# Kernel optimization log

Measured on AMD Instinct MI355X. Metric: run time of the kernel, lower is better.

## Reference

```python
import jax, jax.numpy as jnp
import numpy as np

NEG = -9.0e15

def gat_layer(X, adj_mask, W, Wb, a1, a2, ab):
    # X: [N, Fin]; W: [Fin, Fout]; a1,a2: [Fout]; ab: scalar
    h = X @ W + Wb                                   # [N, Fout]
    # a([h_i || h_j]) = h_i@a1 + h_j@a2 + ab  (decomposition of concat+linear)
    e = jax.nn.leaky_relu((h @ a1)[:, None] + (h @ a2)[None, :] + ab,
                          negative_slope=0.2)        # [N, N]
    e = jnp.where(adj_mask, e, NEG)
    attn = jax.nn.softmax(e, axis=1)                 # [N, N]
    return jax.nn.elu(attn @ h)                      # [N, Fout]

def setup_inputs() -> dict:
    key = jax.random.key(0)
    ks = jax.random.split(key, 12)
    N, Fin, Fh, H, Fout = 4096, 512, 128, 4, 64
    X = jax.random.normal(ks[0], (N, Fin), dtype=jnp.float32)
    adjacency_matrix = jax.random.randint(ks[1], (N, N), 0, 2, dtype=jnp.int32)
    s_in = 1.0 / np.sqrt(Fin)
    s_a = 1.0 / np.sqrt(2 * Fh)
    W_h  = jax.random.uniform(ks[2], (H, Fin, Fh), jnp.float32, -s_in, s_in)
    b_h  = jax.random.uniform(ks[3], (H, Fh), jnp.float32, -s_in, s_in)
    a1_h = jax.random.uniform(ks[4], (H, Fh), jnp.float32, -s_a, s_a)
    a2_h = jax.random.uniform(ks[5], (H, Fh), jnp.float32, -s_a, s_a)
    ab_h = jax.random.uniform(ks[6], (H,), jnp.float32, -s_a, s_a)
    Fcat = H * Fh
    s_c = 1.0 / np.sqrt(Fcat)
    s_ao = 1.0 / np.sqrt(2 * Fout)
    W_o  = jax.random.uniform(ks[7], (Fcat, Fout), jnp.float32, -s_c, s_c)
    b_o  = jax.random.uniform(ks[8], (Fout,), jnp.float32, -s_c, s_c)
    a1_o = jax.random.uniform(ks[9], (Fout,), jnp.float32, -s_ao, s_ao)
    a2_o = jax.random.uniform(ks[10], (Fout,), jnp.float32, -s_ao, s_ao)
    ab_o = jax.random.uniform(ks[11], (), jnp.float32, -s_ao, s_ao)
    return {"X": X, "adjacency_matrix": adjacency_matrix,
            "W_h": W_h, "b_h": b_h, "a1_h": a1_h, "a2_h": a2_h, "ab_h": ab_h,
            "W_o": W_o, "b_o": b_o, "a1_o": a1_o, "a2_o": a2_o, "ab_o": ab_o}

def reference(X, adjacency_matrix, W_h, b_h, a1_h, a2_h, ab_h,
              W_o, b_o, a1_o, a2_o, ab_o):
    adj_mask = adjacency_matrix > 0
    # per-head attention layers, vmapped over heads
    heads = jax.vmap(gat_layer, in_axes=(None, None, 0, 0, 0, 0, 0))(
        X, adj_mask, W_h, b_h, a1_h, a2_h, ab_h)      # [H, N, Fh]
    H, N, Fh = heads.shape
    x = jnp.transpose(heads, (1, 0, 2)).reshape(N, H * Fh)  # concat along features
    x = gat_layer(x, adj_mask, W_o, b_o, a1_o, a2_o, ab_o)  # [N, Fout]
    return jax.nn.log_softmax(x, axis=1)
```

## Files before the change

### kernel.cpp

```cpp
#include <hip/hip_runtime.h>
#include <math.h>

#define NN 4096

using f32x4  = __attribute__((ext_vector_type(4))) float;
using bf16x4 = __attribute__((ext_vector_type(4))) __bf16;
using bf16x8 = __attribute__((ext_vector_type(8))) __bf16;

__device__ __forceinline__ void barrier_lgkm() {
    asm volatile("s_waitcnt lgkmcnt(0)\ns_barrier" ::: "memory");
}

template<int FH>
__device__ __forceinline__ void stage_tile(const __bf16* __restrict__ hgp,
                                           __bf16* dst, int tid) {
#pragma unroll
    for (int it = 0; it < FH / 32; it++) {
        int c = tid + it * 256;
        int f = c >> 3, sl = c & 7;
        int g = sl ^ (f & 7);
        __builtin_amdgcn_global_load_lds(
            (const __attribute__((address_space(1))) void*)(hgp + (size_t)f * NN + g * 8),
            (__attribute__((address_space(3))) void*)(dst + (size_t)c * 8), 16, 0, 0);
    }
}

__device__ __forceinline__ void stage_g(const __bf16* __restrict__ base, int ldk,
                                        __bf16* dst, int tid) {
#pragma unroll
    for (int it = 0; it < 2; it++) {
        int c = tid + it * 256;
        int f = c >> 3, sl = c & 7;
        int g = sl ^ (f & 7);
        __builtin_amdgcn_global_load_lds(
            (const __attribute__((address_space(1))) void*)(base + (size_t)f * ldk + g * 8),
            (__attribute__((address_space(3))) void*)(dst + (size_t)c * 8), 16, 0, 0);
    }
}

__global__ void pack_adj_kernel(const int* __restrict__ adj,
                                unsigned long long* __restrict__ bits) {
    int gw = (blockIdx.x * blockDim.x + threadIdx.x) >> 6;
    int lane = threadIdx.x & 63;
    int v = adj[(size_t)gw * 64 + lane];
    unsigned long long m = __ballot(v > 0);
    if (lane == 0) bits[gw] = m;
}

__global__ void prepack_kernel(const float* __restrict__ W_h, const float* __restrict__ b_h,
                               const float* __restrict__ W_o,
                               __bf16* __restrict__ Bt1, float* __restrict__ biasp,
                               __bf16* __restrict__ Bt2) {
    int idx = blockIdx.x * 256 + threadIdx.x;
    {
        int n = idx >> 9, k = idx & 511;
        int h = n >> 7, f = n & 127;
        Bt1[idx] = (__bf16)W_h[(size_t)h * 512 * 128 + k * 128 + f];
    }
    if (idx < 64 * 512) {
        int n = idx >> 9, k = idx & 511;
        Bt2[idx] = (__bf16)W_o[k * 64 + n];
    }
    if (idx < 512) biasp[idx] = b_h[idx];
}

__global__ void cast_bf16_kernel(const float* __restrict__ src, __bf16* __restrict__ dst) {
    int i = blockIdx.x * 256 + threadIdx.x;
    f32x4 v = *(const f32x4*)(src + (size_t)i * 4);
    bf16x4 o;
#pragma unroll
    for (int q = 0; q < 4; q++) o[q] = (__bf16)v[q];
    *(bf16x4*)(dst + (size_t)i * 4) = o;
}

__global__ __launch_bounds__(256) void gemm_fused_kernel(
    const __bf16* __restrict__ A, const __bf16* __restrict__ Bt,
    const float* __restrict__ bias,
    const float* __restrict__ a1, const float* __restrict__ a2,
    __bf16* __restrict__ Ht, float* __restrict__ s1, float* __restrict__ s2,
    int M, int N, int K)
{
    __shared__ __attribute__((aligned(16))) __bf16 As[2][64 * 64];
    __shared__ __attribute__((aligned(16))) __bf16 Bs[2][64 * 64];
    const int tid = threadIdx.x, w = tid >> 6, l = tid & 63, o = l >> 4, rl = l & 15;
    const int bm = blockIdx.y * 64, bn = blockIdx.x * 64;
    f32x4 acc[4] = {};
    stage_g(A + (size_t)bm * K, K, &As[0][0], tid);
    stage_g(Bt + (size_t)bn * K, K, &Bs[0][0], tid);
    const int KB = K / 64;
    for (int kb = 0; kb < KB; kb++) {
        int b = kb & 1;
        __syncthreads();
        if (kb + 1 < KB) {
            stage_g(A + (size_t)bm * K + (kb + 1) * 64, K, &As[b ^ 1][0], tid);
            stage_g(Bt + (size_t)bn * K + (kb + 1) * 64, K, &Bs[b ^ 1][0], tid);
        }
#pragma unroll
        for (int kt = 0; kt < 2; kt++) {
            int ra = w * 16 + rl;
            int cg = kt * 4 + o;
            bf16x8 af = *(const bf16x8*)(&As[b][(ra * 8 + (cg ^ (ra & 7))) * 8]);
#pragma unroll
            for (int nt = 0; nt < 4; nt++) {
                int rb = nt * 16 + rl;
                bf16x8 bfr = *(const bf16x8*)(&Bs[b][(rb * 8 + (cg ^ (rb & 7))) * 8]);
                acc[nt] = __builtin_amdgcn_mfma_f32_16x16x32_bf16(af, bfr, acc[nt], 0, 0, 0);
            }
        }
    }
    const int head = bn >> 7;
    const int row_base = bm + w * 16 + o * 4;
    float p1[4] = {0.f, 0.f, 0.f, 0.f}, p2[4] = {0.f, 0.f, 0.f, 0.f};
#pragma unroll
    for (int nt = 0; nt < 4; nt++) {
        int col = bn + nt * 16 + rl;
        float bv = bias[col];
        float a1v = a1[col], a2v = a2[col];
        bf16x4 hv;
#pragma unroll
        for (int r4 = 0; r4 < 4; r4++) {
            float h = acc[nt][r4] + bv;
            hv[r4] = (__bf16)h;
            p1[r4] += h * a1v;
            p2[r4] += h * a2v;
        }
        *(bf16x4*)(Ht + (size_t)col * M + row_base) = hv;
    }
#pragma unroll
    for (int r4 = 0; r4 < 4; r4++)
#pragma unroll
        for (int off = 1; off < 16; off <<= 1) {
            p1[r4] += __shfl_xor(p1[r4], off, 64);
            p2[r4] += __shfl_xor(p2[r4], off, 64);
        }
    if (rl == 0)
#pragma unroll
        for (int r4 = 0; r4 < 4; r4++) {
            atomicAdd(&s1[(size_t)head * M + row_base + r4], p1[r4]);
            atomicAdd(&s2[(size_t)head * M + row_base + r4], p2[r4]);
        }
}

__global__ void smax_kernel(const float* __restrict__ s2, float* __restrict__ s2max) {
    const float* p = s2 + (size_t)blockIdx.x * NN;
    int t = threadIdx.x;
    float m = -INFINITY;
    for (int i = t; i < NN; i += 256) m = fmaxf(m, p[i]);
#pragma unroll
    for (int off = 1; off < 64; off <<= 1) m = fmaxf(m, __shfl_xor(m, off, 64));
    __shared__ float red[4];
    if ((t & 63) == 0) red[t >> 6] = m;
    __syncthreads();
    if (t == 0) s2max[blockIdx.x] = fmaxf(fmaxf(red[0], red[1]), fmaxf(red[2], red[3]));
}

template<int FH, int JSPLIT>
__global__ __launch_bounds__(256, 4) void attn_kernel(
    const __bf16* __restrict__ Htg,
    const unsigned long long* __restrict__ adj_bits,
    const float* __restrict__ s1_all, const float* __restrict__ s2_all,
    const float* __restrict__ s2max_all, const float* __restrict__ ab_all,
    __bf16* __restrict__ accp,
    float* __restrict__ lg,
    int ldo)
{
    constexpr int NJT = NN / 64 / JSPLIT;
    constexpr int NTW = FH / 64;
    const int head = blockIdx.y;
    const int js   = blockIdx.z;
    const int row0 = blockIdx.x * 64;
    const int jt0  = js * NJT;
    const int tid = threadIdx.x;
    const int w = tid >> 6, l = tid & 63, o = l >> 4, rl = l & 15;
    const int myrow = row0 + w * 16 + rl;

    __shared__ __attribute__((aligned(16))) __bf16 hbuf[2][FH * 64];
    __shared__ __attribute__((aligned(16))) __bf16 plds[8 * 64 * 8];

    const float* s2 = s2_all + (size_t)head * NN;
    const __bf16* hg = Htg + (size_t)head * FH * NN;
    const float s1r = s1_all[(size_t)head * NN + myrow] + ab_all[head];
    float mrow; { float x = s1r + s2max_all[head]; mrow = fmaxf(x, 0.2f * x); }
    float lacc = 0.f;
    f32x4 acc[4][NTW] = {};

    stage_tile<FH>(hg + (size_t)jt0 * 64, &hbuf[0][0], tid);

    for (int jl = 0; jl < NJT; jl++) {
        const int b = jl & 1;
        const int jt = jt0 + jl;
        unsigned long long aw = adj_bits[(size_t)myrow * 64 + jt];
        bf16x8 freg[2];
#pragma unroll
        for (int kt = 0; kt < 2; kt++) {
            unsigned int mbyte = (unsigned int)(aw >> ((kt * 4 + o) * 8)) & 0xFFu;
            int jb = jt * 64 + kt * 32 + o * 8;
            f32x4 sa = *(const f32x4*)(s2 + jb);
            f32x4 sb = *(const f32x4*)(s2 + jb + 4);
            float ps = 0.f;
#pragma unroll
            for (int q = 0; q < 8; q++) {
                float s2q = (q < 4) ? sa[q] : sb[q - 4];
                float x = s1r + s2q;
                float e = fmaxf(x, 0.2f * x);
                float p = ((mbyte >> q) & 1u) ? __expf(e - mrow) : 0.f;
                freg[kt][q] = (__bf16)p;
                ps += p;
            }
            ps += __shfl_xor(ps, 16, 64);
            ps += __shfl_xor(ps, 32, 64);
            lacc += ps;
            *(bf16x8*)(&plds[((w * 2 + kt) * 64 + l) * 8]) = freg[kt];
        }
        __syncthreads();
        if (jl + 1 < NJT)
            stage_tile<FH>(hg + (size_t)(jt + 1) * 64, &hbuf[b ^ 1][0], tid);
        bf16x8 bfr[2][NTW];
#pragma unroll
        for (int kt = 0; kt < 2; kt++)
#pragma unroll
            for (int ntl = 0; ntl < NTW; ntl++) {
                int f = (w * NTW + ntl) * 16 + rl;
                int slot = (kt * 4 + o) ^ (rl & 7);
                bfr[kt][ntl] = *(const bf16x8*)(&hbuf[b][(f * 8 + slot) * 8]);
            }
#pragma unroll
        for (int mt = 0; mt < 4; mt++)
#pragma unroll
            for (int kt = 0; kt < 2; kt++) {
                bf16x8 af = (mt == w) ? freg[kt]
                          : *(const bf16x8*)(&plds[((mt * 2 + kt) * 64 + l) * 8]);
#pragma unroll
                for (int ntl = 0; ntl < NTW; ntl++)
                    acc[mt][ntl] = __builtin_amdgcn_mfma_f32_16x16x32_bf16(
                        af, bfr[kt][ntl], acc[mt][ntl], 0, 0, 0);
            }
        barrier_lgkm();
    }
    if (l < 16) lg[((size_t)head * JSPLIT + js) * NN + row0 + w * 16 + l] = lacc;
#pragma unroll
    for (int mt = 0; mt < 4; mt++)
#pragma unroll
        for (int ntl = 0; ntl < NTW; ntl++)
#pragma unroll
            for (int r4 = 0; r4 < 4; r4++) {
                int grow = row0 + mt * 16 + o * 4 + r4;
                int gcol = head * FH + (w * NTW + ntl) * 16 + rl;
                accp[((size_t)js * NN + grow) * ldo + gcol] = (__bf16)acc[mt][ntl][r4];
            }
}

__global__ void combine1_kernel(const __bf16* __restrict__ accp, const float* __restrict__ lg,
                                __bf16* __restrict__ outb) {
    int gid = blockIdx.x * 256 + threadIdx.x;
    int row = gid >> 7, c4 = (gid & 127) * 4;
    int head = c4 >> 7;
    float lsum = 0.f;
#pragma unroll
    for (int js = 0; js < 4; js++) lsum += lg[((size_t)head * 4 + js) * NN + row];
    float inv = lsum > 0.f ? 1.f / lsum : 0.f;
    float v[4] = {0.f, 0.f, 0.f, 0.f};
#pragma unroll
    for (int js = 0; js < 4; js++) {
        bf16x4 t = *(const bf16x4*)(accp + ((size_t)js * NN + row) * 512 + c4);
#pragma unroll
        for (int q = 0; q < 4; q++) v[q] += (float)t[q];
    }
    bf16x4 ob;
#pragma unroll
    for (int q = 0; q < 4; q++) {
        float x = v[q] * inv;
        x = x > 0.f ? x : __expf(x) - 1.f;
        ob[q] = (__bf16)x;
    }
    *(bf16x4*)(outb + (size_t)row * 512 + c4) = ob;
}

__global__ void combine2_kernel(const __bf16* __restrict__ accp, const float* __restrict__ lg,
                                float* __restrict__ out) {
    int row = (blockIdx.x * 256 + threadIdx.x) >> 6;
    int lane = threadIdx.x & 63;
    if (row >= NN) return;
    float lsum = 0.f, v = 0.f;
#pragma unroll
    for (int js = 0; js < 16; js++) {
        lsum += lg[(size_t)js * NN + row];
        v += (float)accp[((size_t)js * NN + row) * 64 + lane];
    }
    float inv = lsum > 0.f ? 1.f / lsum : 0.f;
    v *= inv;
    v = v > 0.f ? v : __expf(v) - 1.f;
    float m = v;
#pragma unroll
    for (int off = 1; off < 64; off <<= 1) m = fmaxf(m, __shfl_xor(m, off, 64));
    float ex = __expf(v - m);
    float s = ex;
#pragma unroll
    for (int off = 1; off < 64; off <<= 1) s += __shfl_xor(s, off, 64);
    out[(size_t)row * 64 + lane] = v - m - __logf(s);
}

extern "C" void kernel_launch(void* const* d_in, const int* in_sizes, int n_in,
                              void* d_out, int out_size, void* d_ws, size_t ws_size,
                              hipStream_t stream) {
    const float* X    = (const float*)d_in[0];
    const int*   adj  = (const int*)d_in[1];
    const float* W_h  = (const float*)d_in[2];
    const float* b_h  = (const float*)d_in[3];
    const float* a1_h = (const float*)d_in[4];
    const float* a2_h = (const float*)d_in[5];
    const float* ab_h = (const float*)d_in[6];
    const float* W_o  = (const float*)d_in[7];
    const float* b_o  = (const float*)d_in[8];
    const float* a1_o = (const float*)d_in[9];
    const float* a2_o = (const float*)d_in[10];
    const float* ab_o = (const float*)d_in[11];
    float* out = (float*)d_out;

    char* ws = (char*)d_ws;
    auto alloc = [&](size_t bytes) {
        char* p = ws; ws += (bytes + 255) & ~(size_t)255; return p;
    };
    unsigned long long* adj_bits = (unsigned long long*)alloc((size_t)NN * 64 * 8);
    __bf16* Bt1    = (__bf16*)alloc((size_t)512 * 512 * 2);
    float*  biasp  = (float*)alloc(512 * 4);
    __bf16* Bt2    = (__bf16*)alloc((size_t)64 * 512 * 2);
    __bf16* Xb     = (__bf16*)alloc((size_t)NN * 512 * 2);
    float*  s1h    = (float*)alloc((size_t)4 * NN * 4);
    float*  s2h    = (float*)alloc((size_t)4 * NN * 4);
    float*  s1o    = (float*)alloc((size_t)NN * 4);
    float*  s2o    = (float*)alloc((size_t)NN * 4);
    float*  s2maxh = (float*)alloc(4 * 4);
    float*  s2maxo = (float*)alloc(4);
    __bf16* Htg    = (__bf16*)alloc((size_t)512 * NN * 2);
    __bf16* accp1  = (__bf16*)alloc((size_t)4 * NN * 512 * 2);
    float*  lg1    = (float*)alloc((size_t)16 * NN * 4);
    __bf16* outhb  = (__bf16*)alloc((size_t)NN * 512 * 2);
    __bf16* Ht2    = (__bf16*)alloc((size_t)64 * NN * 2);
    __bf16* accp2  = (__bf16*)alloc((size_t)16 * NN * 64 * 2);
    float*  lg2    = (float*)alloc((size_t)16 * NN * 4);

    hipMemsetAsync(s1h, 0, (size_t)(4 + 4 + 1 + 1) * NN * 4, stream);
    pack_adj_kernel<<<(NN * 64) / 4, 256, 0, stream>>>(adj, adj_bits);
    prepack_kernel<<<1024, 256, 0, stream>>>(W_h, b_h, W_o, Bt1, biasp, Bt2);
    cast_bf16_kernel<<<(NN * 512 / 4) / 256, 256, 0, stream>>>(X, Xb);
    gemm_fused_kernel<<<dim3(8, 64), 256, 0, stream>>>(
        Xb, Bt1, biasp, a1_h, a2_h, Htg, s1h, s2h, NN, 512, 512);
    smax_kernel<<<4, 256, 0, stream>>>(s2h, s2maxh);
    attn_kernel<128, 4><<<dim3(NN / 64, 4, 4), 256, 0, stream>>>(
        Htg, adj_bits, s1h, s2h, s2maxh, ab_h, accp1, lg1, 512);
    combine1_kernel<<<(NN * 128) / 256, 256, 0, stream>>>(accp1, lg1, outhb);
    gemm_fused_kernel<<<dim3(1, 64), 256, 0, stream>>>(
        outhb, Bt2, b_o, a1_o, a2_o, Ht2, s1o, s2o, NN, 64, 512);
    smax_kernel<<<1, 256, 0, stream>>>(s2o, s2maxo);
    attn_kernel<64, 16><<<dim3(NN / 64, 1, 16), 256, 0, stream>>>(
        Ht2, adj_bits, s1o, s2o, s2maxo, ab_o, accp2, lg2, 64);
    combine2_kernel<<<(NN * 64) / 256, 256, 0, stream>>>(accp2, lg2, out);
}
```

Measured before the change: 228.8 us.

## Software-pipeline attention probability generation with MFMA and use exp2 with prescaled scores

The attention kernel now computes the masked exp probabilities for the next key tile before issuing the current tile's MFMAs, so VALU exp work can overlap with matrix instructions. Scores are pre-scaled by log2(e) in the projection kernel (a1, a2 and ab), which lets the exp be done with a native exp2 instead of __expf. Masking uses a large negative exponent instead of a select after the exp, and the elementwise ops use packed float2 vectors. This adds register pressure from holding a second set of probability fragments, which may lower occupancy.

```diff
diff --git a/kernel.cpp b/kernel.cpp
--- a/kernel.cpp
+++ b/kernel.cpp
@@ -2,10 +2,18 @@
 #include <math.h>
 
 #define NN 4096
-
+#define LOG2E 1.44269504088896340736f
+
+using f32x2  = __attribute__((ext_vector_type(2))) float;
 using f32x4  = __attribute__((ext_vector_type(4))) float;
 using bf16x4 = __attribute__((ext_vector_type(4))) __bf16;
 using bf16x8 = __attribute__((ext_vector_type(8))) __bf16;
+
+#if __has_builtin(__builtin_amdgcn_exp2f)
+#define EXP2(x) __builtin_amdgcn_exp2f(x)
+#else
+#define EXP2(x) __expf((x) * 0.6931471805599453f)
+#endif
 
 __device__ __forceinline__ void barrier_lgkm() {
     asm volatile("s_waitcnt lgkmcnt(0)\ns_barrier" ::: "memory");
@@ -115,7 +123,7 @@
     for (int nt = 0; nt < 4; nt++) {
         int col = bn + nt * 16 + rl;
         float bv = bias[col];
-        float a1v = a1[col], a2v = a2[col];
+        float a1v = a1[col] * LOG2E, a2v = a2[col] * LOG2E;
         bf16x4 hv;
 #pragma unroll
         for (int r4 = 0; r4 < 4; r4++) {
@@ -179,39 +187,53 @@
 
     const float* s2 = s2_all + (size_t)head * NN;
     const __bf16* hg = Htg + (size_t)head * FH * NN;
-    const float s1r = s1_all[(size_t)head * NN + myrow] + ab_all[head];
+    const float s1r = s1_all[(size_t)head * NN + myrow] + ab_all[head] * LOG2E;
     float mrow; { float x = s1r + s2max_all[head]; mrow = fmaxf(x, 0.2f * x); }
     float lacc = 0.f;
     f32x4 acc[4][NTW] = {};
 
     stage_tile<FH>(hg + (size_t)jt0 * 64, &hbuf[0][0], tid);
 
+    auto produce = [&](int jt, bf16x8* fr) {
+        unsigned long long aw = adj_bits[(size_t)myrow * 64 + jt];
+#pragma unroll
+        for (int kt = 0; kt < 2; kt++) {
+            unsigned int mbyte = (unsigned int)(aw >> ((kt * 4 + o) * 8)) & 0xFFu;
+            const float* sp = s2 + jt * 64 + kt * 32 + o * 8;
+            f32x4 sa = *(const f32x4*)(sp);
+            f32x4 sb = *(const f32x4*)(sp + 4);
+            float ps = 0.f;
+#pragma unroll
+            for (int qp = 0; qp < 4; qp++) {
+                f32x2 sv;
+                sv[0] = (qp < 2) ? sa[qp * 2]     : sb[qp * 2 - 4];
+                sv[1] = (qp < 2) ? sa[qp * 2 + 1] : sb[qp * 2 - 3];
+                f32x2 x = sv + s1r;
+                f32x2 e = __builtin_elementwise_max(x, 0.2f * x) - mrow;
+#pragma unroll
+                for (int h2 = 0; h2 < 2; h2++) {
+                    int q = qp * 2 + h2;
+                    float t = ((mbyte >> q) & 1u) ? e[h2] : -1.0e20f;
+                    float p = EXP2(t);
+                    fr[kt][q] = (__bf16)p;
+                    ps += p;
+                }
+            }
+            ps += __shfl_xor(ps, 16, 64);
+            ps += __shfl_xor(ps, 32, 64);
+            lacc += ps;
+        }
+    };
+
+    bf16x8 freg[2];
+    produce(jt0, freg);
+
     for (int jl = 0; jl < NJT; jl++) {
         const int b = jl & 1;
         const int jt = jt0 + jl;
-        unsigned long long aw = adj_bits[(size_t)myrow * 64 + jt];
-        bf16x8 freg[2];
-#pragma unroll
-        for (int kt = 0; kt < 2; kt++) {
-            unsigned int mbyte = (unsigned int)(aw >> ((kt * 4 + o) * 8)) & 0xFFu;
-            int jb = jt * 64 + kt * 32 + o * 8;
-            f32x4 sa = *(const f32x4*)(s2 + jb);
-            f32x4 sb = *(const f32x4*)(s2 + jb + 4);
-            float ps = 0.f;
-#pragma unroll
-            for (int q = 0; q < 8; q++) {
-                float s2q = (q < 4) ? sa[q] : sb[q - 4];
-                float x = s1r + s2q;
-                float e = fmaxf(x, 0.2f * x);
-                float p = ((mbyte >> q) & 1u) ? __expf(e - mrow) : 0.f;
-                freg[kt][q] = (__bf16)p;
-                ps += p;
-            }
-            ps += __shfl_xor(ps, 16, 64);
-            ps += __shfl_xor(ps, 32, 64);
-            lacc += ps;
+#pragma unroll
+        for (int kt = 0; kt < 2; kt++)
             *(bf16x8*)(&plds[((w * 2 + kt) * 64 + l) * 8]) = freg[kt];
-        }
         __syncthreads();
         if (jl + 1 < NJT)
             stage_tile<FH>(hg + (size_t)(jt + 1) * 64, &hbuf[b ^ 1][0], tid);
@@ -224,6 +246,8 @@
                 int slot = (kt * 4 + o) ^ (rl & 7);
                 bfr[kt][ntl] = *(const bf16x8*)(&hbuf[b][(f * 8 + slot) * 8]);
             }
+        bf16x8 fnext[2];
+        if (jl + 1 < NJT) produce(jt + 1, fnext);
 #pragma unroll
         for (int mt = 0; mt < 4; mt++)
 #pragma unroll
@@ -236,6 +260,7 @@
                         af, bfr[kt][ntl], acc[mt][ntl], 0, 0, 0);
             }
         barrier_lgkm();
+        if (jl + 1 < NJT) { freg[0] = fnext[0]; freg[1] = fnext[1]; }
     }
     if (l < 16) lg[((size_t)head * JSPLIT + js) * NN + row0 + w * 16 + l] = lacc;
 #pragma unroll
```

New measurement: 228.0 us. Within noise of the previous version (-0.3%).
